# Performance work log

Hardware: AMD Instinct MI355X
Metric: run time of the kernel (lower is better)

Reference implementation:

```python
import math
import jax, jax.numpy as jnp
from jax import lax
import numpy as np

TWO_PI = 2.0 * math.pi
CG_ITERS = 30      # DifferentiableLinearSolver(max_iter=30)
CG_TOL = 1e-6
CG_REG = 1e-6      # reg = 1e-6 * I added inside the solver


def build_second_diff_matrix(N, dtype):
    e = jnp.ones(N, dtype)
    e2 = -2.0 * e
    e2 = e2.at[0].set(-1.0).at[-1].set(-1.0)
    oper = jnp.diag(e2) + jnp.diag(e[:-1], -1) + jnp.diag(e[:-1], 1)
    return oper.T @ oper


def cumtrapz(y, dx):
    # cumulative trapezoid along last axis, keeping length (leading zero)
    avg = (y[..., :-1] + y[..., 1:]) * (0.5 * dx)
    c = jnp.cumsum(avg, axis=-1)
    return jnp.concatenate([jnp.zeros_like(y[..., :1]), c], axis=-1)


def differ5(y, delta):
    mid = (y[..., 2:] - y[..., :-2]) / (2.0 * delta)
    first = (y[..., 1:2] - y[..., 0:1]) / delta
    last = (y[..., -1:] - y[..., -2:-1]) / delta
    return jnp.concatenate([first, mid, last], axis=-1)


def projec5(vec, var):
    # per-row norm-ball projection; vec: (B, N)
    M = vec.shape[-1]
    e = jnp.sqrt(M * var)
    n = jnp.linalg.norm(vec, axis=-1, keepdims=True)
    scale = jnp.where(n > e, e / jnp.maximum(n, 1e-30), 1.0)
    return vec * scale


def cg_solve(opedoub, coef, diagv, rhs, x0):
    # Solves (coef*opedoub + diag(diagv) + CG_REG*I) x = rhs via CG,
    # matching torch semantics (early break freezes state).
    def mv(p):
        return coef * (opedoub @ p) + (diagv + CG_REG) * p

    r0 = rhs - mv(x0)
    rs0 = jnp.dot(r0, r0)

    def step(carry, _):
        x, r, p, rsold, done = carry
        Ap = mv(p)
        a = rsold / (jnp.dot(p, Ap) + 1e-12)
        x1 = jnp.where(done, x, x + a * p)
        r1 = jnp.where(done, r, r - a * Ap)
        rsnew = jnp.dot(r1, r1)
        done1 = done | (jnp.sqrt(rsnew) < CG_TOL)
        bta = rsnew / (rsold + 1e-12)
        p1 = jnp.where(done1, p, r1 + bta * p)
        rsold1 = jnp.where(done1, rsold, rsnew)
        return (x1, r1, p1, rsold1, done1), None

    (x, _, _, _, _), _ = lax.scan(step, (x0, r0, r0, rs0, jnp.array(False)), None, length=CG_ITERS)
    return x


def _forward(s, eIF, xm, ym, sum_x, sum_y, lamuda, init_freqs, mode_mask,
             alpha, beta, var, fs, iteration,
             fe_w1, fe_b1, fe_w2, fe_b2,
             pr_w1, pr_b1, pr_w2, pr_b2, pr_w3, pr_b3, iter_weight):
    dtype = s.dtype
    B, N = s.shape
    K = eIF.shape[1]

    # ---- hyperparameter refinement MLP ----
    avg = jnp.mean(init_freqs, axis=1, keepdims=True)              # (B,1)
    h = jax.nn.relu(avg @ fe_w1.T + fe_b1)
    h = jax.nn.relu(h @ fe_w2.T + fe_b2)                            # (B,16)
    cur = jnp.stack([jnp.broadcast_to(alpha, (B,)),
                     jnp.broadcast_to(beta, (B,))], axis=1)         # (B,2)
    z = jnp.concatenate([h, cur], axis=1)                           # (B,18)
    z = jax.nn.relu(z @ pr_w1.T + pr_b1)
    z = jax.nn.relu(z @ pr_w2.T + pr_b2)
    res = jnp.tanh(z @ pr_w3.T + pr_b3)                             # (B,2)
    fac = jax.nn.sigmoid(iter_weight * iteration)
    res = res * fac * 0.1
    new_alpha = jnp.clip(alpha + jnp.mean(res[:, 0] * alpha), 1e-6, 0.01)
    new_beta = jnp.clip(beta + jnp.mean(res[:, 1] * beta), 1e-6, 0.1)

    betathr = jnp.minimum(10.0 ** (iteration / 36.0 - 10.0), new_beta)
    opedoub = build_second_diff_matrix(N, dtype)
    dx = 1.0 / fs

    # Within the torch k-loop, temp sums / lamuda / new_eIF[b,k] all still hold
    # their *input* values, so all (b,k) sub-problems are independent -> vmap.
    u = projec5(s - sum_x - sum_y - lamuda / new_alpha, var)        # (B,N)

    phase = TWO_PI * cumtrapz(eIF, dx)                               # (B,K,N)
    cosm = jnp.cos(phase)
    sinm = jnp.sin(phase)
    resid = (s[:, None, :] - (sum_x[:, None, :] - xm * cosm)
             - (sum_y[:, None, :] - ym * sinm)
             - u[:, None, :] - (lamuda / new_alpha)[:, None, :])
    rhs_x = cosm * resid
    rhs_y = sinm * resid

    coefA = 2.0 / new_alpha
    flat = lambda t: t.reshape(B * K, N)
    cg_v = jax.vmap(cg_solve, in_axes=(None, None, 0, 0, 0))

    xs = cg_v(opedoub, coefA, flat(cosm ** 2), flat(rhs_x), flat(xm)).reshape(B, K, N)
    ys = cg_v(opedoub, coefA, flat(sinm ** 2), flat(rhs_y), flat(ym)).reshape(B, K, N)

    xbar = differ5(xs, dx)
    ybar = differ5(ys, dx)
    denom = xs ** 2 + ys ** 2 + 1e-12
    deltaIF = (xs * ybar - ys * xbar) / (denom * TWO_PI)

    coefS = 2.0 / betathr
    ones_d = jnp.ones((B * K, N), dtype)
    zeros_d = jnp.zeros((B * K, N), dtype)
    smooth = cg_v(opedoub, coefS, ones_d, flat(deltaIF), zeros_d).reshape(B, K, N)
    eIF_s = eIF - 0.5 * smooth

    active = (mode_mask != 0)[:, :, None]                            # (B,K,1)
    new_xm = jnp.where(active, xs, xm)
    new_ym = jnp.where(active, ys, ym)
    new_eIF = jnp.where(active, eIF_s, eIF)

    new_phase = TWO_PI * cumtrapz(new_eIF, dx)
    maskf = active.astype(dtype)
    bsx = jnp.sum(maskf * new_xm * jnp.cos(new_phase), axis=1)       # (B,N)
    bsy = jnp.sum(maskf * new_ym * jnp.sin(new_phase), axis=1)
    new_lamuda = lamuda + new_alpha * (u + bsx + bsy - s)

    return (new_eIF, new_xm, new_ym, bsx, bsy, new_lamuda, new_alpha, new_beta)


def setup_inputs() -> dict:
    key = jax.random.key(0)
    B, K, N = 8, 4, 2048
    ks = jax.random.split(key, 20)
    f32 = jnp.float32
    inp = {
        "s": jax.random.normal(ks[0], (B, N), f32),
        "eIF": 50.0 + 200.0 * jax.random.uniform(ks[1], (B, K, N), f32),
        "xm": 0.1 * jax.random.normal(ks[2], (B, K, N), f32),
        "ym": 0.1 * jax.random.normal(ks[3], (B, K, N), f32),
        "sum_x": 0.1 * jax.random.normal(ks[4], (B, N), f32),
        "sum_y": 0.1 * jax.random.normal(ks[5], (B, N), f32),
        "lamuda": 0.01 * jax.random.normal(ks[6], (B, N), f32),
        "init_freqs": 50.0 + 200.0 * jax.random.uniform(ks[7], (B, K), f32),
        "mode_mask": jnp.ones((B, K), jnp.int32),
        "alpha": jnp.asarray(0.005, f32),
        "beta": jnp.asarray(0.05, f32),
        "var": jnp.asarray(0.01, f32),
        "fs": jnp.asarray(2000.0, f32),
        "iteration": 1,
        # HyperparameterRefinement params (torch Linear: y = x @ W.T + b)
        "fe_w1": 0.1 * jax.random.normal(ks[8], (32, 1), f32),
        "fe_b1": jnp.zeros((32,), f32),
        "fe_w2": 0.1 * jax.random.normal(ks[9], (16, 32), f32),
        "fe_b2": jnp.zeros((16,), f32),
        "pr_w1": 0.1 * jax.random.normal(ks[10], (64, 18), f32),
        "pr_b1": jnp.zeros((64,), f32),
        "pr_w2": 0.1 * jax.random.normal(ks[11], (32, 64), f32),
        "pr_b2": jnp.zeros((32,), f32),
        "pr_w3": 0.1 * jax.random.normal(ks[12], (2, 32), f32),
        "pr_b3": jnp.zeros((2,), f32),
        "iter_weight": jnp.asarray(0.1, f32),
    }
    return inp


def reference(s, eIF, xm, ym, sum_x, sum_y, lamuda, init_freqs, mode_mask,
              alpha, beta, var, fs, iteration,
              fe_w1, fe_b1, fe_w2, fe_b2,
              pr_w1, pr_b1, pr_w2, pr_b2, pr_w3, pr_b3, iter_weight):
    return _forward(s, eIF, xm, ym, sum_x, sum_y, lamuda, init_freqs, mode_mask,
                    alpha, beta, var, fs, iteration,
                    fe_w1, fe_b1, fe_w2, fe_b2,
                    pr_w1, pr_b1, pr_w2, pr_b2, pr_w3, pr_b3, iter_weight)
```

## Files before the change

### kernel.cpp

```cpp
#include <hip/hip_runtime.h>
#include <math.h>

#define Nq 2048
#define Bq 8
#define Kq 4
#define BKq 32
#define NL 32
#define NP 16
#define TWO_PI_D 6.283185307179586
#define PI_D 3.141592653589793
#define INV2PI_D 0.15915494309189535

typedef float v2f __attribute__((ext_vector_type(2)));

__device__ __forceinline__ v2f mk2(float a, float b) {
  v2f r; r.x = a; r.y = b; return r;
}


__device__ __forceinline__ double wave_sum_d(double v) {
#pragma unroll
  for (int off = 1; off < 64; off <<= 1) v += __shfl_xor(v, off, 64);
  return v;
}

__device__ __forceinline__ float dpp_sum_f32(float v) {
  v += __int_as_float(__builtin_amdgcn_update_dpp(0, __float_as_int(v), 0x111, 0xf, 0xf, false));
  v += __int_as_float(__builtin_amdgcn_update_dpp(0, __float_as_int(v), 0x112, 0xf, 0xf, false));
  v += __int_as_float(__builtin_amdgcn_update_dpp(0, __float_as_int(v), 0x114, 0xf, 0xe, false));
  v += __int_as_float(__builtin_amdgcn_update_dpp(0, __float_as_int(v), 0x118, 0xf, 0xc, false));
  v += __int_as_float(__builtin_amdgcn_update_dpp(0, __float_as_int(v), 0x142, 0xa, 0xf, false));
  v += __int_as_float(__builtin_amdgcn_update_dpp(0, __float_as_int(v), 0x143, 0xc, 0xf, false));
  return __int_as_float(__builtin_amdgcn_readlane(__float_as_int(v), 63));
}

__device__ __forceinline__ float dpp_shr1(float v) {
  return __int_as_float(__builtin_amdgcn_update_dpp(0, __float_as_int(v), 0x138, 0xf, 0xf, false));
}
__device__ __forceinline__ float dpp_shl1(float v) {
  return __int_as_float(__builtin_amdgcn_update_dpp(0, __float_as_int(v), 0x130, 0xf, 0xf, false));
}

__device__ __forceinline__ double lane_excl_prefix_d(double T, int lane) {
  double acc = T;
#pragma unroll
  for (int off = 1; off < 64; off <<= 1) {
    double t = __shfl_up(acc, off, 64);
    if (lane >= off) acc += t;
  }
  return acc - T;
}

__device__ __forceinline__ void fast_sincos_ph(double ph, float* sn, float* cs) {
  double k = trunc(ph * INV2PI_D);
  float phr = (float)(ph - k * TWO_PI_D);
  __sincosf(phr, sn, cs);
}

template <bool UNIT_DIAG, bool ZERO_X0>
__device__ __forceinline__ void cg_wave_pk(float coef, const v2f* De, float deu,
                                           v2f* R, v2f* X, int lane) {
  v2f P[NP], AP[NP];

  auto applyA = [&](const v2f* V) {
    float lm2 = dpp_shr1(V[NP - 1].x);
    float lm1 = dpp_shr1(V[NP - 1].y);
    float rp1 = dpp_shl1(V[0].x);
    float rp2 = dpp_shl1(V[0].y);
    v2f Vm = mk2(lm2, lm1);
    v2f Vp = mk2(rp1, rp2);
#pragma unroll
    for (int j = 0; j < NP; ++j) {
      v2f Vprev = (j == 0) ? Vm : V[j - 1];
      v2f Vnext = (j == NP - 1) ? Vp : V[j + 1];
      v2f t = Vprev + Vnext;
      t += V[j] * 6.0f;
      float m1x = Vprev.y + V[j].y;
      float m1y = V[j].x + Vnext.x;
      t.x -= 4.0f * m1x;
      t.y -= 4.0f * m1y;
      v2f de = UNIT_DIAG ? mk2(deu, deu) : De[j];
      AP[j] = t * coef + de * V[j];
    }
    if (lane == 0) {
      AP[0].x += coef * (V[0].y - 4.0f * V[0].x);
      AP[0].y += coef * V[0].x;
    }
    if (lane == 63) {
      AP[NP - 1].x += coef * V[NP - 1].y;
      AP[NP - 1].y += coef * (V[NP - 1].x - 4.0f * V[NP - 1].y);
    }
  };

  float rsold, inv_rsold;
  {
    if (!ZERO_X0) {
      applyA(X);
#pragma unroll
      for (int j = 0; j < NP; ++j) R[j] -= AP[j];
    }
    v2f a0 = mk2(0.f, 0.f), a1 = mk2(0.f, 0.f);
#pragma unroll
    for (int j = 0; j < NP; j += 2) {
      P[j] = R[j];
      a0 += R[j] * R[j];
      P[j + 1] = R[j + 1];
      a1 += R[j + 1] * R[j + 1];
    }
    v2f s = a0 + a1;
    rsold = dpp_sum_f32(s.x + s.y);
    inv_rsold = __builtin_amdgcn_rcpf(rsold + 1e-12f);
  }

  for (int it = 0; it < 30; ++it) {
    applyA(P);
    v2f a0 = mk2(0.f, 0.f), a1 = mk2(0.f, 0.f);
#pragma unroll
    for (int j = 0; j < NP; j += 2) {
      a0 += P[j] * AP[j];
      a1 += P[j + 1] * AP[j + 1];
    }
    v2f s = a0 + a1;
    float pap = dpp_sum_f32(s.x + s.y);
    float a = rsold * __builtin_amdgcn_rcpf(pap + 1e-12f);
    v2f r0 = mk2(0.f, 0.f), r1 = mk2(0.f, 0.f);
#pragma unroll
    for (int j = 0; j < NP; j += 2) {
      X[j] += P[j] * a;
      R[j] -= AP[j] * a;
      r0 += R[j] * R[j];
      X[j + 1] += P[j + 1] * a;
      R[j + 1] -= AP[j + 1] * a;
      r1 += R[j + 1] * R[j + 1];
    }
    v2f t = r0 + r1;
    float rsnew = dpp_sum_f32(t.x + t.y);
    if (rsnew < 1e-12f) break;
    float bta = rsnew * inv_rsold;
#pragma unroll
    for (int j = 0; j < NP; ++j) P[j] = R[j] + P[j] * bta;
    rsold = rsnew;
    inv_rsold = __builtin_amdgcn_rcpf(rsnew + 1e-12f);
  }
}

__global__ __launch_bounds__(128, 1) void row_kernel(
    const float* __restrict__ s, const float* __restrict__ eIF,
    const float* __restrict__ xm, const float* __restrict__ ym,
    const float* __restrict__ sum_x, const float* __restrict__ sum_y,
    const float* __restrict__ lamuda, const float* __restrict__ init_freqs,
    const int* __restrict__ mode_mask, const float* __restrict__ alpha_p,
    const float* __restrict__ beta_p, const float* __restrict__ var_p,
    const float* __restrict__ fs_p, const int* __restrict__ iter_p,
    const float* __restrict__ fe_w1, const float* __restrict__ fe_b1,
    const float* __restrict__ fe_w2, const float* __restrict__ fe_b2,
    const float* __restrict__ pr_w1, const float* __restrict__ pr_b1,
    const float* __restrict__ pr_w2, const float* __restrict__ pr_b2,
    const float* __restrict__ pr_w3, const float* __restrict__ pr_b3,
    const float* __restrict__ iter_w_p, double* __restrict__ hdr,
    float* __restrict__ out_eIF, float* __restrict__ out_xm,
    float* __restrict__ out_ym, float* __restrict__ cx_w,
    float* __restrict__ cy_w, float* __restrict__ out_scal) {
  __shared__ double sh_avg[Bq];
  __shared__ double sh_h1[Bq][32];
  __shared__ double sh_z[Bq][18];
  __shared__ double sh_z1[Bq][64];
  __shared__ double sh_z2[Bq][32];
  __shared__ double sh_res[Bq][2];
  __shared__ double sh_hdr[6];
  __shared__ float sh_xs[Nq], sh_ys[Nq];

  const int tid = threadIdx.x;
  const int wv = tid >> 6, lane = tid & 63;
  const int row = blockIdx.x, b = row >> 2;
  const int bb = b * Nq, base = row * Nq;

  double alpha = (double)alpha_p[0], beta = (double)beta_p[0];
  double iterv = (double)iter_p[0];
  if (tid < Bq) {
    double avg = 0.0;
#pragma unroll
    for (int k = 0; k < Kq; ++k) avg += (double)init_freqs[tid * Kq + k];
    sh_avg[tid] = avg * (1.0 / Kq);
  }
  __syncthreads();
  for (int n = tid; n < 256; n += 128) {
    int b2 = n >> 5, j = n & 31;
    double v = (double)fe_w1[j] * sh_avg[b2] + (double)fe_b1[j];
    sh_h1[b2][j] = v > 0.0 ? v : 0.0;
  }
  __syncthreads();
  {
    int b2 = tid >> 4, j = tid & 15;
    double acc = (double)fe_b2[j];
    for (int i = 0; i < 32; ++i) acc += (double)fe_w2[j * 32 + i] * sh_h1[b2][i];
    sh_z[b2][j] = acc > 0.0 ? acc : 0.0;
  }
  if (tid < Bq) {
    sh_z[tid][16] = alpha;
    sh_z[tid][17] = beta;
  }
  __syncthreads();
  for (int n = tid; n < 512; n += 128) {
    int b2 = n >> 6, j = n & 63;
    double acc = (double)pr_b1[j];
    for (int i = 0; i < 18; ++i) acc += (double)pr_w1[j * 18 + i] * sh_z[b2][i];
    sh_z1[b2][j] = acc > 0.0 ? acc : 0.0;
  }
  __syncthreads();
  for (int n = tid; n < 256; n += 128) {
    int b2 = n >> 5, j = n & 31;
    double acc = (double)pr_b2[j];
    for (int i = 0; i < 64; ++i) acc += (double)pr_w2[j * 64 + i] * sh_z1[b2][i];
    sh_z2[b2][j] = acc > 0.0 ? acc : 0.0;
  }
  __syncthreads();
  if (tid < 16) {
    int b2 = tid >> 1, c = tid & 1;
    double acc = (double)pr_b3[c];
    for (int i = 0; i < 32; ++i) acc += (double)pr_w3[c * 32 + i] * sh_z2[b2][i];
    double fac = 1.0 / (1.0 + exp(-(double)iter_w_p[0] * iterv));
    sh_res[b2][c] = tanh(acc) * fac * 0.1;
  }
  __syncthreads();
  if (tid == 0) {
    double r0 = 0.0, r1 = 0.0;
    for (int q = 0; q < Bq; ++q) { r0 += sh_res[q][0]; r1 += sh_res[q][1]; }
    double na = fmin(fmax(alpha + r0 * alpha * (1.0 / Bq), 1e-6), 0.01);
    double nb = fmin(fmax(beta + r1 * beta * (1.0 / Bq), 1e-6), 0.1);
    double betathr = fmin(pow(10.0, iterv / 36.0 - 10.0), nb);
    sh_hdr[0] = na;
    sh_hdr[1] = 2.0 / na;
    sh_hdr[2] = 2.0 / betathr;
    sh_hdr[3] = 1.0 / na;
    hdr[0] = na;
    hdr[4] = 1.0 / na;
    out_scal[0] = (float)na;
    out_scal[1] = (float)nb;
  }
  __syncthreads();
  const float coefA = (float)sh_hdr[1];
  const float coefS = (float)sh_hdr[2];
  const double inva = sh_hdr[3];

  double tv[NL];
  {
    const float4* S4 = reinterpret_cast<const float4*>(s + bb);
    const float4* SX4 = reinterpret_cast<const float4*>(sum_x + bb);
    const float4* SY4 = reinterpret_cast<const float4*>(sum_y + bb);
    const float4* L4 = reinterpret_cast<const float4*>(lamuda + bb);
    double n0 = 0.0, n1 = 0.0;
#pragma unroll
    for (int q = 0; q < 8; ++q) {
      float4 av = S4[lane * 8 + q];
      float4 bv = SX4[lane * 8 + q];
      float4 cv = SY4[lane * 8 + q];
      float4 dv = L4[lane * 8 + q];
      int e = 4 * q;
      tv[e + 0] = (double)av.x - (double)bv.x - (double)cv.x - (double)dv.x * inva;
      tv[e + 1] = (double)av.y - (double)bv.y - (double)cv.y - (double)dv.y * inva;
      tv[e + 2] = (double)av.z - (double)bv.z - (double)cv.z - (double)dv.z * inva;
      tv[e + 3] = (double)av.w - (double)bv.w - (double)cv.w - (double)dv.w * inva;
      n0 += tv[e + 0] * tv[e + 0];
      n1 += tv[e + 1] * tv[e + 1];
      n0 += tv[e + 2] * tv[e + 2];
      n1 += tv[e + 3] * tv[e + 3];
    }
    double nsq = wave_sum_d(n0 + n1);
    double nn = sqrt(nsq);
    double ee = sqrt((double)Nq * (double)var_p[0]);
    double scale = (nn > ee) ? ee / fmax(nn, 1e-30) : 1.0;
    if (tid == 0 && (row & 3) == 0) hdr[8 + b] = scale;
    double oms = 1.0 - scale;
#pragma unroll
    for (int e = 0; e < NL; ++e) tv[e] *= oms;
  }

  const double dx = 1.0 / (double)fs_p[0];
  const double c0 = PI_D * dx;
  v2f De[NP], R[NP], X[NP];
  {
    double ev[NL], pl[NL];
    const float4* E4 = reinterpret_cast<const float4*>(eIF + base);
#pragma unroll
    for (int q = 0; q < 8; ++q) {
      float4 e4 = E4[lane * 8 + q];
      ev[4 * q + 0] = (double)e4.x;
      ev[4 * q + 1] = (double)e4.y;
      ev[4 * q + 2] = (double)e4.z;
      ev[4 * q + 3] = (double)e4.w;
    }
    pl[0] = ev[0];
#pragma unroll
    for (int e = 1; e < NL; ++e) pl[e] = pl[e - 1] + ev[e];
    double offs = lane_excl_prefix_d(pl[NL - 1], lane);
    double y0 = __shfl(ev[0], 0, 64);
    const float4* XM4 = reinterpret_cast<const float4*>(xm + base);
    const float4* YM4 = reinterpret_cast<const float4*>(ym + base);
#pragma unroll
    for (int q = 0; q < 8; ++q) {
      float4 xm4 = XM4[lane * 8 + q];
      float4 ym4 = YM4[lane * 8 + q];
      float xa[4] = {xm4.x, xm4.y, xm4.z, xm4.w};
      float ya[4] = {ym4.x, ym4.y, ym4.z, ym4.w};
#pragma unroll
      for (int t2 = 0; t2 < 4; ++t2) {
        int e = 4 * q + t2;
        double ph = c0 * (2.0 * (offs + pl[e]) - ev[e] - y0);
        float sn, cs;
        fast_sincos_ph(ph, &sn, &cs);
        float xmv = xa[t2], ymv = ya[t2];
        double resid = tv[e] + (double)xmv * (double)cs + (double)ymv * (double)sn;
        float trig = (wv == 0) ? cs : sn;
        float de = trig * trig + 1e-6f;
        float rr = (float)((double)trig * resid);
        float xx = (wv == 0) ? xmv : ymv;
        int j = e >> 1;
        if (e & 1) {
          De[j].y = de; R[j].y = rr; X[j].y = xx;
        } else {
          De[j].x = de; R[j].x = rr; X[j].x = xx;
        }
      }
    }
  }

  cg_wave_pk<false, false>(coefA, De, 0.0f, R, X, lane);

  {
    float* dst = (wv == 0) ? sh_xs : sh_ys;
#pragma unroll
    for (int e = 0; e < NL; ++e) {
      float xv = (e & 1) ? X[e >> 1].y : X[e >> 1].x;
      dst[e * 64 + lane] = xv;
    }
  }
  __syncthreads();

  {
    float xs[NL], ys[NL];
#pragma unroll
    for (int e = 0; e < NL; ++e) {
      xs[e] = sh_xs[e * 64 + lane];
      ys[e] = sh_ys[e * 64 + lane];
    }
    float invdx = (float)fs_p[0], inv2dx = 0.5f * invdx;
    float xl = dpp_shr1(xs[NL - 1]), xr = dpp_shl1(xs[0]);
    float yl = dpp_shr1(ys[NL - 1]), yr = dpp_shl1(ys[0]);
#pragma unroll
    for (int e = 0; e < NL; ++e) {
      int i = lane * NL + e;
      float xm1 = (e >= 1) ? xs[e - 1] : xl;
      float xp1 = (e <= NL - 2) ? xs[e + 1] : xr;
      float ym1 = (e >= 1) ? ys[e - 1] : yl;
      float yp1 = (e <= NL - 2) ? ys[e + 1] : yr;
      float xb, yb;
      if (i == 0) {
        xb = (xp1 - xs[e]) * invdx;
        yb = (yp1 - ys[e]) * invdx;
      } else if (i == Nq - 1) {
        xb = (xs[e] - xm1) * invdx;
        yb = (ys[e] - ym1) * invdx;
      } else {
        xb = (xp1 - xm1) * inv2dx;
        yb = (yp1 - ym1) * inv2dx;
      }
      float denom = xs[e] * xs[e] + ys[e] * ys[e] + 1e-12f;
      float rr = (xs[e] * yb - ys[e] * xb) / (denom * (float)TWO_PI_D);
      int j = e >> 1;
      if (e & 1) {
        R[j].y = rr; X[j].y = 0.0f;
      } else {
        R[j].x = rr; X[j].x = 0.0f;
      }
    }
  }

  cg_wave_pk<true, true>(coefS, nullptr, 1.0f + 1e-6f, R, X, lane);

  bool active = mode_mask[row] != 0;
  double eifn[NL], pl[NL];
#pragma unroll
  for (int e = 0; e < NL; ++e) {
    int i = base + lane * NL + e;
    double eifv = (double)eIF[i];
    double sm = (double)((e & 1) ? X[e >> 1].y : X[e >> 1].x);
    eifn[e] = active ? (eifv - 0.5 * sm) : eifv;
  }
  if (wv == 0) {
#pragma unroll
    for (int e = 0; e < NL; ++e) {
      int i = base + lane * NL + e;
      out_eIF[i] = (float)eifn[e];
      out_xm[i] = active ? sh_xs[e * 64 + lane] : xm[i];
    }
  } else {
#pragma unroll
    for (int e = 0; e < NL; ++e) {
      int i = base + lane * NL + e;
      out_ym[i] = active ? sh_ys[e * 64 + lane] : ym[i];
    }
  }
  pl[0] = eifn[0];
#pragma unroll
  for (int e = 1; e < NL; ++e) pl[e] = pl[e - 1] + eifn[e];
  double offs = lane_excl_prefix_d(pl[NL - 1], lane);
  double y0 = __shfl(eifn[0], 0, 64);
#pragma unroll
  for (int e = 0; e < NL; ++e) {
    int i = base + lane * NL + e;
    double ph = c0 * (2.0 * (offs + pl[e]) - eifn[e] - y0);
    float sn, cs;
    fast_sincos_ph(ph, &sn, &cs);
    if (wv == 0)
      cx_w[i] = active ? sh_xs[e * 64 + lane] * cs : 0.0f;
    else
      cy_w[i] = active ? sh_ys[e * 64 + lane] * sn : 0.0f;
  }
}

__global__ __launch_bounds__(128) void final_kernel(
    const float* __restrict__ s, const float* __restrict__ sum_x,
    const float* __restrict__ sum_y, const float* __restrict__ lamuda,
    const double* __restrict__ hdr, const float* __restrict__ cx_w,
    const float* __restrict__ cy_w, float* __restrict__ out_bsx,
    float* __restrict__ out_bsy, float* __restrict__ out_lam) {
  int gi = blockIdx.x * 128 + threadIdx.x;
  int b = gi >> 11, i = gi & (Nq - 1);
  double na = hdr[0], inva = hdr[4], scale = hdr[8 + b];
  double sv = (double)s[gi];
  double t = sv - (double)sum_x[gi] - (double)sum_y[gi] -
             (double)lamuda[gi] * inva;
  double bx = 0.0, by = 0.0;
#pragma unroll
  for (int k = 0; k < Kq; ++k) {
    bx += (double)cx_w[(b * Kq + k) * Nq + i];
    by += (double)cy_w[(b * Kq + k) * Nq + i];
  }
  double u = t * scale;
  double nl = (double)lamuda[gi] + na * (u + bx + by - sv);
  out_bsx[gi] = (float)bx;
  out_bsy[gi] = (float)by;
  out_lam[gi] = (float)nl;
}

extern "C" void kernel_launch(void* const* d_in, const int* in_sizes, int n_in,
                              void* d_out, int out_size, void* d_ws, size_t ws_size,
                              hipStream_t stream) {
  (void)in_sizes; (void)n_in; (void)out_size; (void)ws_size;
  const float* s = (const float*)d_in[0];
  const float* eIF = (const float*)d_in[1];
  const float* xm = (const float*)d_in[2];
  const float* ym = (const float*)d_in[3];
  const float* sum_x = (const float*)d_in[4];
  const float* sum_y = (const float*)d_in[5];
  const float* lamuda = (const float*)d_in[6];
  const float* init_freqs = (const float*)d_in[7];
  const int* mode_mask = (const int*)d_in[8];
  const float* alpha = (const float*)d_in[9];
  const float* beta = (const float*)d_in[10];
  const float* var = (const float*)d_in[11];
  const float* fs = (const float*)d_in[12];
  const int* iteration = (const int*)d_in[13];
  const float* fe_w1 = (const float*)d_in[14];
  const float* fe_b1 = (const float*)d_in[15];
  const float* fe_w2 = (const float*)d_in[16];
  const float* fe_b2 = (const float*)d_in[17];
  const float* pr_w1 = (const float*)d_in[18];
  const float* pr_b1 = (const float*)d_in[19];
  const float* pr_w2 = (const float*)d_in[20];
  const float* pr_b2 = (const float*)d_in[21];
  const float* pr_w3 = (const float*)d_in[22];
  const float* pr_b3 = (const float*)d_in[23];
  const float* iter_weight = (const float*)d_in[24];

  float* out = (float*)d_out;
  const int BN = Bq * Nq;
  const int BKN = BKq * Nq;
  float* out_eIF = out;
  float* out_xm = out + BKN;
  float* out_ym = out + 2 * BKN;
  float* out_bsx = out + 3 * BKN;
  float* out_bsy = out + 3 * BKN + BN;
  float* out_lam = out + 3 * BKN + 2 * BN;
  float* out_scal = out + 3 * BKN + 3 * BN;

  double* W = (double*)d_ws;
  double* hdr = W;
  float* F = (float*)(W + 16);
  float* cx_w = F;
  float* cy_w = F + BKN;

  row_kernel<<<BKq, 128, 0, stream>>>(
      s, eIF, xm, ym, sum_x, sum_y, lamuda, init_freqs, mode_mask, alpha, beta,
      var, fs, iteration, fe_w1, fe_b1, fe_w2, fe_b2, pr_w1, pr_b1, pr_w2,
      pr_b2, pr_w3, pr_b3, iter_weight, hdr, out_eIF, out_xm, out_ym, cx_w,
      cy_w, out_scal);
  final_kernel<<<BN / 128, 128, 0, stream>>>(s, sum_x, sum_y, lamuda, hdr,
                                             cx_w, cy_w, out_bsx, out_bsy,
                                             out_lam);
}
```

Baseline: 158.8 us.

## Split each CG system across two waves and merge per-iteration reductions

Each row's two 2048-element CG solves were each run by a single 64-lane wave. They are now split across two waves per system, in 256-thread blocks. Boundary values of the search direction are exchanged through shared-memory seams, with block barriers each iteration. The residual norm is now derived algebraically from p·Ap and Ap·Ap, so both dot products are reduced together in one paired DPP reduction instead of two sequential ones. The aim is to halve the serial per-wave work in this latency-bound solver, at the cost of two __syncthreads per iteration and a slightly different numerical path for rsnew that may lose precision.

```diff
diff --git a/kernel.cpp b/kernel.cpp
--- a/kernel.cpp
+++ b/kernel.cpp
@@ -5,8 +5,8 @@
 #define Bq 8
 #define Kq 4
 #define BKq 32
-#define NL 32
-#define NP 16
+#define NL2 16
+#define NP2 8
 #define TWO_PI_D 6.283185307179586
 #define PI_D 3.141592653589793
 #define INV2PI_D 0.15915494309189535
@@ -17,6 +17,8 @@
   v2f r; r.x = a; r.y = b; return r;
 }
 
+#define ELEM(A, e) (((e) & 1) ? A[(e) >> 1].y : A[(e) >> 1].x)
+
 
 __device__ __forceinline__ double wave_sum_d(double v) {
 #pragma unroll
@@ -24,14 +26,31 @@
   return v;
 }
 
+template <int CTRL, int RM, int BM>
+__device__ __forceinline__ float dpp_add(float acc, float v) {
+  return acc + __int_as_float(__builtin_amdgcn_update_dpp(
+                   0, __float_as_int(v), CTRL, RM, BM, false));
+}
+
 __device__ __forceinline__ float dpp_sum_f32(float v) {
-  v += __int_as_float(__builtin_amdgcn_update_dpp(0, __float_as_int(v), 0x111, 0xf, 0xf, false));
-  v += __int_as_float(__builtin_amdgcn_update_dpp(0, __float_as_int(v), 0x112, 0xf, 0xf, false));
-  v += __int_as_float(__builtin_amdgcn_update_dpp(0, __float_as_int(v), 0x114, 0xf, 0xe, false));
-  v += __int_as_float(__builtin_amdgcn_update_dpp(0, __float_as_int(v), 0x118, 0xf, 0xc, false));
-  v += __int_as_float(__builtin_amdgcn_update_dpp(0, __float_as_int(v), 0x142, 0xa, 0xf, false));
-  v += __int_as_float(__builtin_amdgcn_update_dpp(0, __float_as_int(v), 0x143, 0xc, 0xf, false));
+  v = dpp_add<0x111, 0xf, 0xf>(v, v);
+  v = dpp_add<0x112, 0xf, 0xf>(v, v);
+  v = dpp_add<0x114, 0xf, 0xe>(v, v);
+  v = dpp_add<0x118, 0xf, 0xc>(v, v);
+  v = dpp_add<0x142, 0xa, 0xf>(v, v);
+  v = dpp_add<0x143, 0xc, 0xf>(v, v);
   return __int_as_float(__builtin_amdgcn_readlane(__float_as_int(v), 63));
+}
+
+__device__ __forceinline__ void dpp_sum2(float& v, float& w) {
+  v = dpp_add<0x111, 0xf, 0xf>(v, v); w = dpp_add<0x111, 0xf, 0xf>(w, w);
+  v = dpp_add<0x112, 0xf, 0xf>(v, v); w = dpp_add<0x112, 0xf, 0xf>(w, w);
+  v = dpp_add<0x114, 0xf, 0xe>(v, v); w = dpp_add<0x114, 0xf, 0xe>(w, w);
+  v = dpp_add<0x118, 0xf, 0xc>(v, v); w = dpp_add<0x118, 0xf, 0xc>(w, w);
+  v = dpp_add<0x142, 0xa, 0xf>(v, v); w = dpp_add<0x142, 0xa, 0xf>(w, w);
+  v = dpp_add<0x143, 0xc, 0xf>(v, v); w = dpp_add<0x143, 0xc, 0xf>(w, w);
+  v = __int_as_float(__builtin_amdgcn_readlane(__float_as_int(v), 63));
+  w = __int_as_float(__builtin_amdgcn_readlane(__float_as_int(w), 63));
 }
 
 __device__ __forceinline__ float dpp_shr1(float v) {
@@ -57,94 +76,125 @@
   __sincosf(phr, sn, cs);
 }
 
-template <bool UNIT_DIAG, bool ZERO_X0>
-__device__ __forceinline__ void cg_wave_pk(float coef, const v2f* De, float deu,
-                                           v2f* R, v2f* X, int lane) {
-  v2f P[NP], AP[NP];
-
-  auto applyA = [&](const v2f* V) {
-    float lm2 = dpp_shr1(V[NP - 1].x);
-    float lm1 = dpp_shr1(V[NP - 1].y);
-    float rp1 = dpp_shl1(V[0].x);
-    float rp2 = dpp_shl1(V[0].y);
-    v2f Vm = mk2(lm2, lm1);
-    v2f Vp = mk2(rp1, rp2);
-#pragma unroll
-    for (int j = 0; j < NP; ++j) {
-      v2f Vprev = (j == 0) ? Vm : V[j - 1];
-      v2f Vnext = (j == NP - 1) ? Vp : V[j + 1];
-      v2f t = Vprev + Vnext;
-      t += V[j] * 6.0f;
-      float m1x = Vprev.y + V[j].y;
-      float m1y = V[j].x + Vnext.x;
-      t.x -= 4.0f * m1x;
-      t.y -= 4.0f * m1y;
-      v2f de = UNIT_DIAG ? mk2(deu, deu) : De[j];
-      AP[j] = t * coef + de * V[j];
-    }
-    if (lane == 0) {
-      AP[0].x += coef * (V[0].y - 4.0f * V[0].x);
-      AP[0].y += coef * V[0].x;
-    }
-    if (lane == 63) {
-      AP[NP - 1].x += coef * V[NP - 1].y;
-      AP[NP - 1].y += coef * (V[NP - 1].x - 4.0f * V[NP - 1].y);
-    }
-  };
-
-  float rsold, inv_rsold;
-  {
-    if (!ZERO_X0) {
-      applyA(X);
-#pragma unroll
-      for (int j = 0; j < NP; ++j) R[j] -= AP[j];
-    }
-    v2f a0 = mk2(0.f, 0.f), a1 = mk2(0.f, 0.f);
-#pragma unroll
-    for (int j = 0; j < NP; j += 2) {
-      P[j] = R[j];
-      a0 += R[j] * R[j];
-      P[j + 1] = R[j + 1];
-      a1 += R[j + 1] * R[j + 1];
-    }
-    v2f s = a0 + a1;
-    rsold = dpp_sum_f32(s.x + s.y);
-    inv_rsold = __builtin_amdgcn_rcpf(rsold + 1e-12f);
-  }
-
+template <bool UD>
+__device__ __forceinline__ void applyA_h(const v2f* V, v2f* AP, float coef,
+                                         const v2f* De, float deu, int lane,
+                                         bool leftB, const float* seam) {
+  float lm2 = dpp_shr1(V[NP2 - 1].x);
+  float lm1 = dpp_shr1(V[NP2 - 1].y);
+  float rp1 = dpp_shl1(V[0].x);
+  float rp2 = dpp_shl1(V[0].y);
+  if (leftB) {
+    if (lane == 63) { rp1 = seam[2]; rp2 = seam[3]; }
+  } else {
+    if (lane == 0) { lm2 = seam[0]; lm1 = seam[1]; }
+  }
+  v2f Vm = mk2(lm2, lm1), Vp = mk2(rp1, rp2);
+#pragma unroll
+  for (int j = 0; j < NP2; ++j) {
+    v2f Vprev = (j == 0) ? Vm : V[j - 1];
+    v2f Vnext = (j == NP2 - 1) ? Vp : V[j + 1];
+    v2f t = Vprev + Vnext;
+    t += V[j] * 6.0f;
+    float m1x = Vprev.y + V[j].y;
+    float m1y = V[j].x + Vnext.x;
+    t.x -= 4.0f * m1x;
+    t.y -= 4.0f * m1y;
+    v2f de = UD ? mk2(deu, deu) : De[j];
+    AP[j] = t * coef + de * V[j];
+  }
+  if (leftB && lane == 0) {
+    AP[0].x += coef * (V[0].y - 4.0f * V[0].x);
+    AP[0].y += coef * V[0].x;
+  }
+  if (!leftB && lane == 63) {
+    AP[NP2 - 1].x += coef * V[NP2 - 1].y;
+    AP[NP2 - 1].y += coef * (V[NP2 - 1].x - 4.0f * V[NP2 - 1].y);
+  }
+}
+
+template <bool UD, bool ZX>
+__device__ __forceinline__ void cg_block(float coef, const v2f* De, float deu,
+                                         v2f* R, v2f* X, int lane, bool leftB,
+                                         float* seam, float* dot2, float* rs0s,
+                                         int h) {
+  v2f P[NP2], AP[NP2];
+  if (!ZX) {
+    if (leftB) {
+      if (lane == 63) { seam[0] = X[NP2 - 1].x; seam[1] = X[NP2 - 1].y; }
+    } else {
+      if (lane == 0) { seam[2] = X[0].x; seam[3] = X[0].y; }
+    }
+    __syncthreads();
+    applyA_h<UD>(X, AP, coef, De, deu, lane, leftB, seam);
+#pragma unroll
+    for (int j = 0; j < NP2; ++j) R[j] -= AP[j];
+    __syncthreads();
+  }
+  float rs = 0.0f;
+#pragma unroll
+  for (int j = 0; j < NP2; ++j) {
+    P[j] = R[j];
+    rs += R[j].x * R[j].x + R[j].y * R[j].y;
+  }
+  rs = dpp_sum_f32(rs);
+  if (lane == 0) rs0s[h] = rs;
+  if (leftB) {
+    if (lane == 63) { seam[0] = P[NP2 - 1].x; seam[1] = P[NP2 - 1].y; }
+  } else {
+    if (lane == 0) { seam[2] = P[0].x; seam[3] = P[0].y; }
+  }
+  __syncthreads();
+  float rsold = rs0s[0] + rs0s[1];
+  float inv_rsold = __builtin_amdgcn_rcpf(rsold + 1e-12f);
+  bool done = false;
   for (int it = 0; it < 30; ++it) {
-    applyA(P);
-    v2f a0 = mk2(0.f, 0.f), a1 = mk2(0.f, 0.f);
-#pragma unroll
-    for (int j = 0; j < NP; j += 2) {
-      a0 += P[j] * AP[j];
-      a1 += P[j + 1] * AP[j + 1];
-    }
-    v2f s = a0 + a1;
-    float pap = dpp_sum_f32(s.x + s.y);
-    float a = rsold * __builtin_amdgcn_rcpf(pap + 1e-12f);
-    v2f r0 = mk2(0.f, 0.f), r1 = mk2(0.f, 0.f);
-#pragma unroll
-    for (int j = 0; j < NP; j += 2) {
-      X[j] += P[j] * a;
-      R[j] -= AP[j] * a;
-      r0 += R[j] * R[j];
-      X[j + 1] += P[j + 1] * a;
-      R[j + 1] -= AP[j + 1] * a;
-      r1 += R[j + 1] * R[j + 1];
-    }
-    v2f t = r0 + r1;
-    float rsnew = dpp_sum_f32(t.x + t.y);
-    if (rsnew < 1e-12f) break;
-    float bta = rsnew * inv_rsold;
-#pragma unroll
-    for (int j = 0; j < NP; ++j) P[j] = R[j] + P[j] * bta;
-    rsold = rsnew;
-    inv_rsold = __builtin_amdgcn_rcpf(rsnew + 1e-12f);
-  }
-}
-
-__global__ __launch_bounds__(128, 1) void row_kernel(
+    if (!done) {
+      applyA_h<UD>(P, AP, coef, De, deu, lane, leftB, seam);
+      float pp = 0.0f, aa = 0.0f;
+#pragma unroll
+      for (int j = 0; j < NP2; ++j) {
+        pp += P[j].x * AP[j].x + P[j].y * AP[j].y;
+        aa += AP[j].x * AP[j].x + AP[j].y * AP[j].y;
+      }
+      dpp_sum2(pp, aa);
+      if (lane == 0) { dot2[h * 2 + 0] = pp; dot2[h * 2 + 1] = aa; }
+    }
+    __syncthreads();
+    if (!done) {
+      float pap = dot2[0] + dot2[2];
+      float apap = dot2[1] + dot2[3];
+      float a = rsold * __builtin_amdgcn_rcpf(pap + 1e-12f);
+      float rsnew = a * (a * apap) - rsold;
+      if (rsnew < 1e-12f) {
+#pragma unroll
+        for (int j = 0; j < NP2; ++j) {
+          X[j] += P[j] * a;
+          R[j] -= AP[j] * a;
+        }
+        done = true;
+      } else {
+        float bta = rsnew * inv_rsold;
+#pragma unroll
+        for (int j = 0; j < NP2; ++j) {
+          X[j] += P[j] * a;
+          R[j] -= AP[j] * a;
+          P[j] = R[j] + P[j] * bta;
+        }
+        rsold = rsnew;
+        inv_rsold = __builtin_amdgcn_rcpf(rsnew + 1e-12f);
+        if (leftB) {
+          if (lane == 63) { seam[0] = P[NP2 - 1].x; seam[1] = P[NP2 - 1].y; }
+        } else {
+          if (lane == 0) { seam[2] = P[0].x; seam[3] = P[0].y; }
+        }
+      }
+    }
+    __syncthreads();
+  }
+}
+
+__global__ __launch_bounds__(256, 1) void row_kernel(
     const float* __restrict__ s, const float* __restrict__ eIF,
     const float* __restrict__ xm, const float* __restrict__ ym,
     const float* __restrict__ sum_x, const float* __restrict__ sum_y,
@@ -168,12 +218,20 @@
   __shared__ double sh_z2[Bq][32];
   __shared__ double sh_res[Bq][2];
   __shared__ double sh_hdr[6];
+  __shared__ double sh_nrm[2][2];
+  __shared__ double sh_ph[2][2];
+  __shared__ float sh_seam[2][4];
+  __shared__ float sh_dot[2][4];
+  __shared__ float sh_rs0[2][2];
   __shared__ float sh_xs[Nq], sh_ys[Nq];
 
   const int tid = threadIdx.x;
   const int wv = tid >> 6, lane = tid & 63;
+  const int sys = wv >> 1, h = wv & 1;
+  const bool leftB = (h == 0);
   const int row = blockIdx.x, b = row >> 2;
   const int bb = b * Nq, base = row * Nq;
+  const int goff = h << 10;
 
   double alpha = (double)alpha_p[0], beta = (double)beta_p[0];
   double iterv = (double)iter_p[0];
@@ -184,13 +242,13 @@
     sh_avg[tid] = avg * (1.0 / Kq);
   }
   __syncthreads();
-  for (int n = tid; n < 256; n += 128) {
-    int b2 = n >> 5, j = n & 31;
+  {
+    int b2 = tid >> 5, j = tid & 31;
     double v = (double)fe_w1[j] * sh_avg[b2] + (double)fe_b1[j];
     sh_h1[b2][j] = v > 0.0 ? v : 0.0;
   }
   __syncthreads();
-  {
+  if (tid < 128) {
     int b2 = tid >> 4, j = tid & 15;
     double acc = (double)fe_b2[j];
     for (int i = 0; i < 32; ++i) acc += (double)fe_w2[j * 32 + i] * sh_h1[b2][i];
@@ -201,15 +259,15 @@
     sh_z[tid][17] = beta;
   }
   __syncthreads();
-  for (int n = tid; n < 512; n += 128) {
+  for (int n = tid; n < 512; n += 256) {
     int b2 = n >> 6, j = n & 63;
     double acc = (double)pr_b1[j];
     for (int i = 0; i < 18; ++i) acc += (double)pr_w1[j * 18 + i] * sh_z[b2][i];
     sh_z1[b2][j] = acc > 0.0 ? acc : 0.0;
   }
   __syncthreads();
-  for (int n = tid; n < 256; n += 128) {
-    int b2 = n >> 5, j = n & 31;
+  {
+    int b2 = tid >> 5, j = tid & 31;
     double acc = (double)pr_b2[j];
     for (int i = 0; i < 64; ++i) acc += (double)pr_w2[j * 64 + i] * sh_z1[b2][i];
     sh_z2[b2][j] = acc > 0.0 ? acc : 0.0;
@@ -242,20 +300,22 @@
   const float coefA = (float)sh_hdr[1];
   const float coefS = (float)sh_hdr[2];
   const double inva = sh_hdr[3];
-
-  double tv[NL];
-  {
-    const float4* S4 = reinterpret_cast<const float4*>(s + bb);
-    const float4* SX4 = reinterpret_cast<const float4*>(sum_x + bb);
-    const float4* SY4 = reinterpret_cast<const float4*>(sum_y + bb);
-    const float4* L4 = reinterpret_cast<const float4*>(lamuda + bb);
+  const double fsv = (double)fs_p[0];
+  const double c0 = PI_D / fsv;
+
+  double tv[NL2];
+  {
+    const float4* S4 = reinterpret_cast<const float4*>(s + bb + goff);
+    const float4* SX4 = reinterpret_cast<const float4*>(sum_x + bb + goff);
+    const float4* SY4 = reinterpret_cast<const float4*>(sum_y + bb + goff);
+    const float4* L4 = reinterpret_cast<const float4*>(lamuda + bb + goff);
     double n0 = 0.0, n1 = 0.0;
 #pragma unroll
-    for (int q = 0; q < 8; ++q) {
-      float4 av = S4[lane * 8 + q];
-      float4 bv = SX4[lane * 8 + q];
-      float4 cv = SY4[lane * 8 + q];
-      float4 dv = L4[lane * 8 + q];
+    for (int q = 0; q < 4; ++q) {
+      float4 av = S4[lane * 4 + q];
+      float4 bv = SX4[lane * 4 + q];
+      float4 cv = SY4[lane * 4 + q];
+      float4 dv = L4[lane * 4 + q];
       int e = 4 * q;
       tv[e + 0] = (double)av.x - (double)bv.x - (double)cv.x - (double)dv.x * inva;
       tv[e + 1] = (double)av.y - (double)bv.y - (double)cv.y - (double)dv.y * inva;
@@ -266,25 +326,26 @@
       n0 += tv[e + 2] * tv[e + 2];
       n1 += tv[e + 3] * tv[e + 3];
     }
-    double nsq = wave_sum_d(n0 + n1);
+    double part = wave_sum_d(n0 + n1);
+    if (lane == 0) sh_nrm[sys][h] = part;
+    __syncthreads();
+    double nsq = sh_nrm[sys][0] + sh_nrm[sys][1];
     double nn = sqrt(nsq);
     double ee = sqrt((double)Nq * (double)var_p[0]);
     double scale = (nn > ee) ? ee / fmax(nn, 1e-30) : 1.0;
     if (tid == 0 && (row & 3) == 0) hdr[8 + b] = scale;
     double oms = 1.0 - scale;
 #pragma unroll
-    for (int e = 0; e < NL; ++e) tv[e] *= oms;
-  }
-
-  const double dx = 1.0 / (double)fs_p[0];
-  const double c0 = PI_D * dx;
-  v2f De[NP], R[NP], X[NP];
-  {
-    double ev[NL], pl[NL];
-    const float4* E4 = reinterpret_cast<const float4*>(eIF + base);
-#pragma unroll
-    for (int q = 0; q < 8; ++q) {
-      float4 e4 = E4[lane * 8 + q];
+    for (int e = 0; e < NL2; ++e) tv[e] *= oms;
+  }
+
+  v2f De[NP2], R[NP2], X[NP2];
+  {
+    double ev[NL2], pl[NL2];
+    const float4* E4 = reinterpret_cast<const float4*>(eIF + base + goff);
+#pragma unroll
+    for (int q = 0; q < 4; ++q) {
+      float4 e4 = E4[lane * 4 + q];
       ev[4 * q + 0] = (double)e4.x;
       ev[4 * q + 1] = (double)e4.y;
       ev[4 * q + 2] = (double)e4.z;
@@ -292,29 +353,36 @@
     }
     pl[0] = ev[0];
 #pragma unroll
-    for (int e = 1; e < NL; ++e) pl[e] = pl[e - 1] + ev[e];
-    double offs = lane_excl_prefix_d(pl[NL - 1], lane);
-    double y0 = __shfl(ev[0], 0, 64);
-    const float4* XM4 = reinterpret_cast<const float4*>(xm + base);
-    const float4* YM4 = reinterpret_cast<const float4*>(ym + base);
-#pragma unroll
-    for (int q = 0; q < 8; ++q) {
-      float4 xm4 = XM4[lane * 8 + q];
-      float4 ym4 = YM4[lane * 8 + q];
+    for (int e = 1; e < NL2; ++e) pl[e] = pl[e - 1] + ev[e];
+    double offs = lane_excl_prefix_d(pl[NL2 - 1], lane);
+    double tot = __shfl(offs + pl[NL2 - 1], 63, 64);
+    if (lane == 0 && h == 0) {
+      sh_ph[sys][0] = tot;
+      sh_ph[sys][1] = ev[0];
+    }
+    __syncthreads();
+    double pre = h ? sh_ph[sys][0] : 0.0;
+    double y0 = sh_ph[sys][1];
+    const float4* XM4 = reinterpret_cast<const float4*>(xm + base + goff);
+    const float4* YM4 = reinterpret_cast<const float4*>(ym + base + goff);
+#pragma unroll
+    for (int q = 0; q < 4; ++q) {
+      float4 xm4 = XM4[lane * 4 + q];
+      float4 ym4 = YM4[lane * 4 + q];
       float xa[4] = {xm4.x, xm4.y, xm4.z, xm4.w};
       float ya[4] = {ym4.x, ym4.y, ym4.z, ym4.w};
 #pragma unroll
       for (int t2 = 0; t2 < 4; ++t2) {
         int e = 4 * q + t2;
-        double ph = c0 * (2.0 * (offs + pl[e]) - ev[e] - y0);
+        double ph = c0 * (2.0 * (pre + offs + pl[e]) - ev[e] - y0);
         float sn, cs;
         fast_sincos_ph(ph, &sn, &cs);
         float xmv = xa[t2], ymv = ya[t2];
         double resid = tv[e] + (double)xmv * (double)cs + (double)ymv * (double)sn;
-        float trig = (wv == 0) ? cs : sn;
+        float trig = (sys == 0) ? cs : sn;
         float de = trig * trig + 1e-6f;
         float rr = (float)((double)trig * resid);
-        float xx = (wv == 0) ? xmv : ymv;
+        float xx = (sys == 0) ? xmv : ymv;
         int j = e >> 1;
         if (e & 1) {
           De[j].y = de; R[j].y = rr; X[j].y = xx;
@@ -325,48 +393,35 @@
     }
   }
 
-  cg_wave_pk<false, false>(coefA, De, 0.0f, R, X, lane);
-
-  {
-    float* dst = (wv == 0) ? sh_xs : sh_ys;
-#pragma unroll
-    for (int e = 0; e < NL; ++e) {
-      float xv = (e & 1) ? X[e >> 1].y : X[e >> 1].x;
-      dst[e * 64 + lane] = xv;
-    }
-  }
-  __syncthreads();
-
-  {
-    float xs[NL], ys[NL];
-#pragma unroll
-    for (int e = 0; e < NL; ++e) {
-      xs[e] = sh_xs[e * 64 + lane];
-      ys[e] = sh_ys[e * 64 + lane];
-    }
-    float invdx = (float)fs_p[0], inv2dx = 0.5f * invdx;
-    float xl = dpp_shr1(xs[NL - 1]), xr = dpp_shl1(xs[0]);
-    float yl = dpp_shr1(ys[NL - 1]), yr = dpp_shl1(ys[0]);
-#pragma unroll
-    for (int e = 0; e < NL; ++e) {
-      int i = lane * NL + e;
-      float xm1 = (e >= 1) ? xs[e - 1] : xl;
-      float xp1 = (e <= NL - 2) ? xs[e + 1] : xr;
-      float ym1 = (e >= 1) ? ys[e - 1] : yl;
-      float yp1 = (e <= NL - 2) ? ys[e + 1] : yr;
+  cg_block<false, false>(coefA, De, 0.0f, R, X, lane, leftB, sh_seam[sys],
+                         sh_dot[sys], sh_rs0[sys], h);
+
+  {
+    float* dst = (sys == 0) ? sh_xs : sh_ys;
+#pragma unroll
+    for (int e = 0; e < NL2; ++e) dst[goff + lane * NL2 + e] = ELEM(X, e);
+  }
+  __syncthreads();
+
+  {
+    float invdx = (float)fsv, inv2dx = 0.5f * invdx;
+#pragma unroll
+    for (int e = 0; e < NL2; ++e) {
+      int i = goff + lane * NL2 + e;
+      float xc = sh_xs[i], yc = sh_ys[i];
       float xb, yb;
       if (i == 0) {
-        xb = (xp1 - xs[e]) * invdx;
-        yb = (yp1 - ys[e]) * invdx;
+        xb = (sh_xs[1] - xc) * invdx;
+        yb = (sh_ys[1] - yc) * invdx;
       } else if (i == Nq - 1) {
-        xb = (xs[e] - xm1) * invdx;
-        yb = (ys[e] - ym1) * invdx;
+        xb = (xc - sh_xs[Nq - 2]) * invdx;
+        yb = (yc - sh_ys[Nq - 2]) * invdx;
       } else {
-        xb = (xp1 - xm1) * inv2dx;
-        yb = (yp1 - ym1) * inv2dx;
+        xb = (sh_xs[i + 1] - sh_xs[i - 1]) * inv2dx;
+        yb = (sh_ys[i + 1] - sh_ys[i - 1]) * inv2dx;
       }
-      float denom = xs[e] * xs[e] + ys[e] * ys[e] + 1e-12f;
-      float rr = (xs[e] * yb - ys[e] * xb) / (denom * (float)TWO_PI_D);
+      float denom = xc * xc + yc * yc + 1e-12f;
+      float rr = (xc * yb - yc * xb) / (denom * (float)TWO_PI_D);
       int j = e >> 1;
       if (e & 1) {
         R[j].y = rr; X[j].y = 0.0f;
@@ -376,46 +431,67 @@
     }
   }
 
-  cg_wave_pk<true, true>(coefS, nullptr, 1.0f + 1e-6f, R, X, lane);
+  cg_block<true, true>(coefS, nullptr, 1.0f + 1e-6f, R, X, lane, leftB,
+                       sh_seam[sys], sh_dot[sys], sh_rs0[sys], h);
 
   bool active = mode_mask[row] != 0;
-  double eifn[NL], pl[NL];
-#pragma unroll
-  for (int e = 0; e < NL; ++e) {
-    int i = base + lane * NL + e;
-    double eifv = (double)eIF[i];
-    double sm = (double)((e & 1) ? X[e >> 1].y : X[e >> 1].x);
-    eifn[e] = active ? (eifv - 0.5 * sm) : eifv;
-  }
-  if (wv == 0) {
-#pragma unroll
-    for (int e = 0; e < NL; ++e) {
-      int i = base + lane * NL + e;
+  double eifn[NL2], pl2[NL2];
+  {
+    const float4* E4 = reinterpret_cast<const float4*>(eIF + base + goff);
+#pragma unroll
+    for (int q = 0; q < 4; ++q) {
+      float4 e4 = E4[lane * 4 + q];
+      double ea[4] = {(double)e4.x, (double)e4.y, (double)e4.z, (double)e4.w};
+#pragma unroll
+      for (int t2 = 0; t2 < 4; ++t2) {
+        int e = 4 * q + t2;
+        double sm = (double)ELEM(X, e);
+        eifn[e] = active ? (ea[t2] - 0.5 * sm) : ea[t2];
+      }
+    }
+  }
+  if (sys == 0) {
+#pragma unroll
+    for (int e = 0; e < NL2; ++e) {
+      int loc = goff + lane * NL2 + e;
+      int i = base + loc;
       out_eIF[i] = (float)eifn[e];
-      out_xm[i] = active ? sh_xs[e * 64 + lane] : xm[i];
+      out_xm[i] = active ? sh_xs[loc] : xm[i];
     }
   } else {
 #pragma unroll
-    for (int e = 0; e < NL; ++e) {
-      int i = base + lane * NL + e;
-      out_ym[i] = active ? sh_ys[e * 64 + lane] : ym[i];
-    }
-  }
-  pl[0] = eifn[0];
-#pragma unroll
-  for (int e = 1; e < NL; ++e) pl[e] = pl[e - 1] + eifn[e];
-  double offs = lane_excl_prefix_d(pl[NL - 1], lane);
-  double y0 = __shfl(eifn[0], 0, 64);
-#pragma unroll
-  for (int e = 0; e < NL; ++e) {
-    int i = base + lane * NL + e;
-    double ph = c0 * (2.0 * (offs + pl[e]) - eifn[e] - y0);
-    float sn, cs;
-    fast_sincos_ph(ph, &sn, &cs);
-    if (wv == 0)
-      cx_w[i] = active ? sh_xs[e * 64 + lane] * cs : 0.0f;
-    else
-      cy_w[i] = active ? sh_ys[e * 64 + lane] * sn : 0.0f;
+    for (int e = 0; e < NL2; ++e) {
+      int loc = goff + lane * NL2 + e;
+      int i = base + loc;
+      out_ym[i] = active ? sh_ys[loc] : ym[i];
+    }
+  }
+  pl2[0] = eifn[0];
+#pragma unroll
+  for (int e = 1; e < NL2; ++e) pl2[e] = pl2[e - 1] + eifn[e];
+  double offs2 = lane_excl_prefix_d(pl2[NL2 - 1], lane);
+  double tot2 = __shfl(offs2 + pl2[NL2 - 1], 63, 64);
+  __syncthreads();
+  if (lane == 0 && h == 0) {
+    sh_ph[sys][0] = tot2;
+    sh_ph[sys][1] = eifn[0];
+  }
+  __syncthreads();
+  {
+    double pre2 = h ? sh_ph[sys][0] : 0.0;
+    double y02 = sh_ph[sys][1];
+#pragma unroll
+    for (int e = 0; e < NL2; ++e) {
+      int loc = goff + lane * NL2 + e;
+      int i = base + loc;
+      double ph = c0 * (2.0 * (pre2 + offs2 + pl2[e]) - eifn[e] - y02);
+      float sn, cs;
+      fast_sincos_ph(ph, &sn, &cs);
+      if (sys == 0)
+        cx_w[i] = active ? sh_xs[loc] * cs : 0.0f;
+      else
+        cy_w[i] = active ? sh_ys[loc] * sn : 0.0f;
+    }
   }
 }
 
@@ -491,7 +567,7 @@
   float* cx_w = F;
   float* cy_w = F + BKN;
 
-  row_kernel<<<BKq, 128, 0, stream>>>(
+  row_kernel<<<BKq, 256, 0, stream>>>(
       s, eIF, xm, ym, sum_x, sum_y, lamuda, init_freqs, mode_mask, alpha, beta,
       var, fs, iteration, fe_w1, fe_b1, fe_w2, fe_b2, pr_w1, pr_b1, pr_w2,
       pr_b2, pr_w3, pr_b3, iter_weight, hdr, out_eIF, out_xm, out_ym, cx_w,
```

New measurement: 169.5 us. +6.7%, slower.
